# Performance work log

Hardware: AMD Instinct MI355X
Metric: run time of the kernel (lower is better)

Reference implementation:

```python
import jax, jax.numpy as jnp
import numpy as np

K = 10
ALPHA = 0.1
BETA = 0.9
GAMMA = BETA ** K + ALPHA * sum(BETA ** i for i in range(K))


def setup_inputs() -> dict:
    key = jax.random.key(0)
    k1, k2, k3 = jax.random.split(key, 3)
    N, D, E = 100000, 256, 1600000
    x = jax.random.normal(k1, (N, D), dtype=jnp.float32)
    edge_weight = jax.random.uniform(k2, (E,), dtype=jnp.float32)
    edge_index = jax.random.randint(k3, (2, E), 0, N, dtype=jnp.int32)
    return {"x": x, "edge_weight": edge_weight, "edge_index": edge_index}


def reference(x, edge_weight, edge_index):
    N = x.shape[0]
    # gcn_norm_adj with renorm: add self-loops (weight 1) then D^-1/2 A D^-1/2
    loops = jnp.arange(N, dtype=edge_index.dtype)
    row = jnp.concatenate([edge_index[0], loops])
    col = jnp.concatenate([edge_index[1], loops])
    w = jnp.concatenate([edge_weight, jnp.ones((N,), dtype=x.dtype)])
    deg = jax.ops.segment_sum(w, row, num_segments=N)
    dinv = jnp.where(deg > 0, jax.lax.rsqrt(deg), 0.0)
    wn = dinv[row] * w * dinv[col]  # normalized edge weights [E+N]

    h = x
    out = h
    for _ in range(K):
        # SpMM: out[r] = sum_e wn[e] * out[col[e]] for row[e]==r
        msg = wn[:, None] * out[col]
        out = jax.ops.segment_sum(msg, row, num_segments=N)
        out = out * BETA + h * ALPHA
    out = out / GAMMA
    return out
```

## Files before the change

### kernel.cpp

```cpp
#include <hip/hip_runtime.h>
#include <hip/hip_fp16.h>
#include <math.h>

#define DFEAT 256
#define KITER 10
#define ALPHA 0.1f
#define BETA 0.9f
#define SCAN_CHUNK 2048


__global__ void count_deg_kernel(const int* __restrict__ row,
                                 const float* __restrict__ w,
                                 float* __restrict__ deg,
                                 int* __restrict__ counts, int E) {
    int e = blockIdx.x * 256 + threadIdx.x;
    if (e < E) {
        int r = row[e];
        atomicAdd(&deg[r], w[e]);
        atomicAdd(&counts[r], 1);
    }
}

__global__ void dinv_kernel(float* __restrict__ deg, int n) {
    int i = blockIdx.x * 256 + threadIdx.x;
    if (i < n) deg[i] = rsqrtf(deg[i] + 1.0f);
}


__global__ __launch_bounds__(256) void scan1_kernel(const int* __restrict__ counts,
                                                    int* __restrict__ row_ptr,
                                                    int* __restrict__ partial, int n) {
    __shared__ int wsum[4];
    int b = blockIdx.x;
    int base = b * SCAN_CHUNK;
    int tid = threadIdx.x;
    int lane = tid & 63, wv = tid >> 6;

    int v[8];
    int s = 0;
    #pragma unroll
    for (int j = 0; j < 8; ++j) {
        int i = base + tid * 8 + j;
        v[j] = (i < n) ? counts[i] : 0;
        s += v[j];
    }
    int incl = s;
    #pragma unroll
    for (int off = 1; off < 64; off <<= 1) {
        int t = __shfl_up(incl, off, 64);
        if (lane >= off) incl += t;
    }
    if (lane == 63) wsum[wv] = incl;
    __syncthreads();
    int woff = 0;
    for (int w = 0; w < wv; ++w) woff += wsum[w];
    int run = woff + incl - s;
    #pragma unroll
    for (int j = 0; j < 8; ++j) {
        int i = base + tid * 8 + j;
        if (i < n) row_ptr[i] = run;
        run += v[j];
    }
    if (tid == 255) partial[b] = run;
}

__global__ void scan2_kernel(int* __restrict__ partial, int nb) {
    __shared__ int tmp[1024];
    int tid = threadIdx.x;
    int v = (tid < nb) ? partial[tid] : 0;
    tmp[tid] = v;
    __syncthreads();
    for (int off = 1; off < 1024; off <<= 1) {
        int t = (tid >= off) ? tmp[tid - off] : 0;
        __syncthreads();
        tmp[tid] += t;
        __syncthreads();
    }
    if (tid < nb) partial[tid] = tmp[tid] - v;
}

__global__ void scan3_kernel(int* __restrict__ row_ptr, int* __restrict__ fill,
                             const int* __restrict__ partial, int n, int E) {
    int i = blockIdx.x * 256 + threadIdx.x;
    if (i < n) {
        int v = row_ptr[i] + partial[i / SCAN_CHUNK];
        row_ptr[i] = v;
        fill[i] = v;
    } else if (i == n) {
        row_ptr[n] = E;
    }
}

__global__ void scatter_kernel(const int* __restrict__ row, const int* __restrict__ col,
                               const float* __restrict__ w, const float* __restrict__ dinv,
                               int* __restrict__ fill, int2* __restrict__ cw, int E) {
    int e = blockIdx.x * 256 + threadIdx.x;
    if (e < E) {
        int r = row[e], c = col[e];
        float wn = dinv[r] * w[e] * dinv[c];
        int pos = atomicAdd(&fill[r], 1);
        cw[pos] = make_int2(c, __float_as_int(wn));
    }
}

__global__ void f2h_kernel(const float* __restrict__ src, __half* __restrict__ dst,
                           size_t n4) {
    size_t i = (size_t)blockIdx.x * 256 + threadIdx.x;
    if (i < n4) {
        float4 v = ((const float4*)src)[i];
        __half2 h0 = __floats2half2_rn(v.x, v.y);
        __half2 h1 = __floats2half2_rn(v.z, v.w);
        float2 o;
        o.x = *reinterpret_cast<float*>(&h0);
        o.y = *reinterpret_cast<float*>(&h1);
        ((float2*)dst)[i] = o;
    }
}

#define ACC(g, wbits) { float wv = __int_as_float(wbits); \
    __half2 h0_ = *reinterpret_cast<__half2*>(&g.x); \
    __half2 h1_ = *reinterpret_cast<__half2*>(&g.y); \
    float2 u0_ = __half22float2(h0_); float2 u1_ = __half22float2(h1_); \
    a0 += wv * u0_.x; a1 += wv * u0_.y; a2 += wv * u1_.x; a3 += wv * u1_.y; }

template<int FINAL>
__global__ __launch_bounds__(256) void spmm_h_kernel(
        const __half* __restrict__ in, const __half* __restrict__ xh,
        float* __restrict__ outf, __half* __restrict__ outh,
        const int* __restrict__ row_ptr, const int2* __restrict__ cw,
        const float* __restrict__ dinv,
        int n, float scale) {
    int wave = threadIdx.x >> 6;
    int lane = threadIdx.x & 63;
    int r = blockIdx.x * 4 + wave;
    if (r >= n) return;

    int start = row_ptr[r];
    int end   = row_ptr[r + 1];
    float dr  = dinv[r];
    float ws  = dr * dr;

    float2 xraw = ((const float2*)(xh + (size_t)r * DFEAT))[lane];

    float2 sraw = ((const float2*)(in + (size_t)r * DFEAT))[lane];
    __half2 s0 = *reinterpret_cast<__half2*>(&sraw.x);
    __half2 s1 = *reinterpret_cast<__half2*>(&sraw.y);
    float2 sf0 = __half22float2(s0), sf1 = __half22float2(s1);
    float a0 = ws * sf0.x, a1 = ws * sf0.y, a2 = ws * sf1.x, a3 = ws * sf1.y;

    int e = start;
    for (; e + 4 <= end; e += 4) {
        int2 p0 = cw[e];
        int2 p1 = cw[e + 1];
        int2 p2 = cw[e + 2];
        int2 p3 = cw[e + 3];
        float2 g0 = ((const float2*)(in + (size_t)p0.x * DFEAT))[lane];
        float2 g1 = ((const float2*)(in + (size_t)p1.x * DFEAT))[lane];
        float2 g2 = ((const float2*)(in + (size_t)p2.x * DFEAT))[lane];
        float2 g3 = ((const float2*)(in + (size_t)p3.x * DFEAT))[lane];
        ACC(g0, p0.y);
        ACC(g1, p1.y);
        ACC(g2, p2.y);
        ACC(g3, p3.y);
    }
    for (; e < end; ++e) {
        int2 p = cw[e];
        float2 g = ((const float2*)(in + (size_t)p.x * DFEAT))[lane];
        ACC(g, p.y);
    }

    __half2 x0 = *reinterpret_cast<__half2*>(&xraw.x);
    __half2 x1 = *reinterpret_cast<__half2*>(&xraw.y);
    float2 xf0 = __half22float2(x0), xf1 = __half22float2(x1);
    float o0 = scale * (BETA * a0 + ALPHA * xf0.x);
    float o1 = scale * (BETA * a1 + ALPHA * xf0.y);
    float o2 = scale * (BETA * a2 + ALPHA * xf1.x);
    float o3 = scale * (BETA * a3 + ALPHA * xf1.y);

    if (FINAL) {
        ((float4*)(outf + (size_t)r * DFEAT))[lane] = make_float4(o0, o1, o2, o3);
    } else {
        __half2 h0 = __floats2half2_rn(o0, o1);
        __half2 h1 = __floats2half2_rn(o2, o3);
        float2 o;
        o.x = *reinterpret_cast<float*>(&h0);
        o.y = *reinterpret_cast<float*>(&h1);
        ((float2*)(outh + (size_t)r * DFEAT))[lane] = o;
    }
}


extern "C" void kernel_launch(void* const* d_in, const int* in_sizes, int n_in,
                              void* d_out, int out_size, void* d_ws, size_t ws_size,
                              hipStream_t stream) {
    const float* x  = (const float*)d_in[0];
    const float* ew = (const float*)d_in[1];
    const int*   ei = (const int*)d_in[2];
    int n = in_sizes[0] / DFEAT;
    int E = in_sizes[1];
    const int* row = ei;
    const int* col = ei + E;
    float* out = (float*)d_out;

    char* ws = (char*)d_ws;
    auto alloc = [&](size_t bytes) {
        char* p = ws;
        ws += (bytes + 255) & ~(size_t)255;
        return p;
    };
    float*  deg     = (float*)alloc((size_t)n * 4);
    int*    counts  = (int*)  alloc((size_t)n * 4);
    int*    row_ptr = (int*)  alloc((size_t)(n + 1) * 4);
    int*    fill    = (int*)  alloc((size_t)n * 4);
    int*    partial = (int*)  alloc((size_t)1024 * 4);
    int2*   cw      = (int2*) alloc((size_t)E * 8);
    __half* xh      = (__half*)alloc((size_t)n * DFEAT * 2);
    __half* H0      = (__half*)alloc((size_t)n * DFEAT * 2);
    __half* H1      = (__half*)d_out;

    hipMemsetAsync(deg, 0, (size_t)n * 4, stream);
    hipMemsetAsync(counts, 0, (size_t)n * 4, stream);

    count_deg_kernel<<<(E + 255) / 256, 256, 0, stream>>>(row, ew, deg, counts, E);
    dinv_kernel<<<(n + 255) / 256, 256, 0, stream>>>(deg, n);

    int nb = (n + SCAN_CHUNK - 1) / SCAN_CHUNK;
    scan1_kernel<<<nb, 256, 0, stream>>>(counts, row_ptr, partial, n);
    scan2_kernel<<<1, 1024, 0, stream>>>(partial, nb);
    scan3_kernel<<<(n + 256) / 256, 256, 0, stream>>>(row_ptr, fill, partial, n, E);

    scatter_kernel<<<(E + 255) / 256, 256, 0, stream>>>(row, col, ew, deg, fill, cw, E);

    size_t n4 = (size_t)n * DFEAT / 4;
    f2h_kernel<<<(int)((n4 + 255) / 256), 256, 0, stream>>>(x, xh, n4);

    double gamma = pow((double)BETA, KITER);
    for (int i = 0; i < KITER; ++i) gamma += (double)ALPHA * pow((double)BETA, i);
    float inv_gamma = (float)(1.0 / gamma);

    int grid = (n + 3) / 4;
    const __half* cur = xh;
    __half* bufs[2] = { H0, H1 };
    for (int k = 0; k < KITER; ++k) {
        if (k < KITER - 1) {
            __half* o = bufs[k & 1];
            spmm_h_kernel<0><<<grid, 256, 0, stream>>>(cur, xh, nullptr, o,
                                                       row_ptr, cw, deg, n, 1.0f);
            cur = o;
        } else {
            spmm_h_kernel<1><<<grid, 256, 0, stream>>>(cur, xh, out, nullptr,
                                                       row_ptr, cw, deg, n, inv_gamma);
        }
    }
}
```

Before: 1.555 ms.

## Pack degree and count atomics, precompute edge ranks, fold normalization into features

A single 64-bit atomic now accumulates both the edge count (upper bits) and a fixed-point weighted degree (lower bits) per row. The value it returns gives each edge its rank within the row, so the CSR scatter no longer needs a second atomic pass or gathers of dinv. The symmetric normalization moves into the feature vectors: the iterate is carried as D^-1/2 times the output, so CSR stores raw edge weights and the scaling by dinv is undone once at the end. The costs are an extra rank array of E ints and fixed-point rounding of the degree sums.

Measured after the change: 1.447 ms. -6.9%, faster.

```diff
diff --git a/kernel.cpp b/kernel.cpp
--- a/kernel.cpp
+++ b/kernel.cpp
@@ -8,26 +8,36 @@
 #define BETA 0.9f
 #define SCAN_CHUNK 2048
 
-
-__global__ void count_deg_kernel(const int* __restrict__ row,
-                                 const float* __restrict__ w,
-                                 float* __restrict__ deg,
-                                 int* __restrict__ counts, int E) {
+#define WSCALE 268435456.0
+#define CNT_SHIFT 40
+
+
+__global__ void edge_pass1_kernel(const int* __restrict__ row,
+                                  const float* __restrict__ w,
+                                  unsigned long long* __restrict__ pk,
+                                  int* __restrict__ rank, int E) {
     int e = blockIdx.x * 256 + threadIdx.x;
     if (e < E) {
         int r = row[e];
-        atomicAdd(&deg[r], w[e]);
-        atomicAdd(&counts[r], 1);
-    }
-}
-
-__global__ void dinv_kernel(float* __restrict__ deg, int n) {
+        unsigned long long add = (1ULL << CNT_SHIFT) |
+            (unsigned long long)((double)w[e] * WSCALE);
+        unsigned long long old = atomicAdd(&pk[r], add);
+        rank[e] = (int)(old >> CNT_SHIFT);
+    }
+}
+
+__global__ void dinv_kernel(const unsigned long long* __restrict__ pk,
+                            float* __restrict__ dinv, int n) {
     int i = blockIdx.x * 256 + threadIdx.x;
-    if (i < n) deg[i] = rsqrtf(deg[i] + 1.0f);
-}
-
-
-__global__ __launch_bounds__(256) void scan1_kernel(const int* __restrict__ counts,
+    if (i < n) {
+        unsigned long long v = pk[i];
+        float deg = (float)((double)(v & ((1ULL << CNT_SHIFT) - 1)) * (1.0 / WSCALE));
+        dinv[i] = rsqrtf(deg + 1.0f);
+    }
+}
+
+
+__global__ __launch_bounds__(256) void scan1_kernel(const unsigned long long* __restrict__ pk,
                                                     int* __restrict__ row_ptr,
                                                     int* __restrict__ partial, int n) {
     __shared__ int wsum[4];
@@ -41,7 +51,7 @@
     #pragma unroll
     for (int j = 0; j < 8; ++j) {
         int i = base + tid * 8 + j;
-        v[j] = (i < n) ? counts[i] : 0;
+        v[j] = (i < n) ? (int)(pk[i] >> CNT_SHIFT) : 0;
         s += v[j];
     }
     int incl = s;
@@ -79,37 +89,36 @@
     if (tid < nb) partial[tid] = tmp[tid] - v;
 }
 
-__global__ void scan3_kernel(int* __restrict__ row_ptr, int* __restrict__ fill,
+__global__ void scan3_kernel(int* __restrict__ row_ptr,
                              const int* __restrict__ partial, int n, int E) {
     int i = blockIdx.x * 256 + threadIdx.x;
     if (i < n) {
-        int v = row_ptr[i] + partial[i / SCAN_CHUNK];
-        row_ptr[i] = v;
-        fill[i] = v;
+        row_ptr[i] += partial[i / SCAN_CHUNK];
     } else if (i == n) {
         row_ptr[n] = E;
     }
 }
 
 __global__ void scatter_kernel(const int* __restrict__ row, const int* __restrict__ col,
-                               const float* __restrict__ w, const float* __restrict__ dinv,
-                               int* __restrict__ fill, int2* __restrict__ cw, int E) {
+                               const float* __restrict__ w, const int* __restrict__ rank,
+                               const int* __restrict__ row_ptr,
+                               int2* __restrict__ cw, int E) {
     int e = blockIdx.x * 256 + threadIdx.x;
     if (e < E) {
-        int r = row[e], c = col[e];
-        float wn = dinv[r] * w[e] * dinv[c];
-        int pos = atomicAdd(&fill[r], 1);
-        cw[pos] = make_int2(c, __float_as_int(wn));
-    }
-}
-
-__global__ void f2h_kernel(const float* __restrict__ src, __half* __restrict__ dst,
-                           size_t n4) {
+        int r = row[e];
+        int pos = row_ptr[r] + rank[e];
+        cw[pos] = make_int2(col[e], __float_as_int(w[e]));
+    }
+}
+
+__global__ void xprime_kernel(const float* __restrict__ x, const float* __restrict__ dinv,
+                              __half* __restrict__ dst, size_t n4) {
     size_t i = (size_t)blockIdx.x * 256 + threadIdx.x;
     if (i < n4) {
-        float4 v = ((const float4*)src)[i];
-        __half2 h0 = __floats2half2_rn(v.x, v.y);
-        __half2 h1 = __floats2half2_rn(v.z, v.w);
+        float4 v = ((const float4*)x)[i];
+        float dr = dinv[i >> 6];
+        __half2 h0 = __floats2half2_rn(dr * v.x, dr * v.y);
+        __half2 h1 = __floats2half2_rn(dr * v.z, dr * v.w);
         float2 o;
         o.x = *reinterpret_cast<float*>(&h0);
         o.y = *reinterpret_cast<float*>(&h1);
@@ -129,7 +138,7 @@
         float* __restrict__ outf, __half* __restrict__ outh,
         const int* __restrict__ row_ptr, const int2* __restrict__ cw,
         const float* __restrict__ dinv,
-        int n, float scale) {
+        int n, float inv_gamma) {
     int wave = threadIdx.x >> 6;
     int lane = threadIdx.x & 63;
     int r = blockIdx.x * 4 + wave;
@@ -138,7 +147,7 @@
     int start = row_ptr[r];
     int end   = row_ptr[r + 1];
     float dr  = dinv[r];
-    float ws  = dr * dr;
+    float c1  = BETA * dr * dr;
 
     float2 xraw = ((const float2*)(xh + (size_t)r * DFEAT))[lane];
 
@@ -146,7 +155,7 @@
     __half2 s0 = *reinterpret_cast<__half2*>(&sraw.x);
     __half2 s1 = *reinterpret_cast<__half2*>(&sraw.y);
     float2 sf0 = __half22float2(s0), sf1 = __half22float2(s1);
-    float a0 = ws * sf0.x, a1 = ws * sf0.y, a2 = ws * sf1.x, a3 = ws * sf1.y;
+    float a0 = sf0.x, a1 = sf0.y, a2 = sf1.x, a3 = sf1.y;
 
     int e = start;
     for (; e + 4 <= end; e += 4) {
@@ -172,13 +181,15 @@
     __half2 x0 = *reinterpret_cast<__half2*>(&xraw.x);
     __half2 x1 = *reinterpret_cast<__half2*>(&xraw.y);
     float2 xf0 = __half22float2(x0), xf1 = __half22float2(x1);
-    float o0 = scale * (BETA * a0 + ALPHA * xf0.x);
-    float o1 = scale * (BETA * a1 + ALPHA * xf0.y);
-    float o2 = scale * (BETA * a2 + ALPHA * xf1.x);
-    float o3 = scale * (BETA * a3 + ALPHA * xf1.y);
+    float o0 = c1 * a0 + ALPHA * xf0.x;
+    float o1 = c1 * a1 + ALPHA * xf0.y;
+    float o2 = c1 * a2 + ALPHA * xf1.x;
+    float o3 = c1 * a3 + ALPHA * xf1.y;
 
     if (FINAL) {
-        ((float4*)(outf + (size_t)r * DFEAT))[lane] = make_float4(o0, o1, o2, o3);
+        float up = inv_gamma / dr;
+        ((float4*)(outf + (size_t)r * DFEAT))[lane] =
+            make_float4(o0 * up, o1 * up, o2 * up, o3 * up);
     } else {
         __half2 h0 = __floats2half2_rn(o0, o1);
         __half2 h1 = __floats2half2_rn(o2, o3);
@@ -208,31 +219,30 @@
         ws += (bytes + 255) & ~(size_t)255;
         return p;
     };
-    float*  deg     = (float*)alloc((size_t)n * 4);
-    int*    counts  = (int*)  alloc((size_t)n * 4);
+    unsigned long long* pk = (unsigned long long*)alloc((size_t)n * 8);
+    int*    rank    = (int*)  alloc((size_t)E * 4);
     int*    row_ptr = (int*)  alloc((size_t)(n + 1) * 4);
-    int*    fill    = (int*)  alloc((size_t)n * 4);
     int*    partial = (int*)  alloc((size_t)1024 * 4);
+    float*  dinv    = (float*)alloc((size_t)n * 4);
     int2*   cw      = (int2*) alloc((size_t)E * 8);
     __half* xh      = (__half*)alloc((size_t)n * DFEAT * 2);
     __half* H0      = (__half*)alloc((size_t)n * DFEAT * 2);
     __half* H1      = (__half*)d_out;
 
-    hipMemsetAsync(deg, 0, (size_t)n * 4, stream);
-    hipMemsetAsync(counts, 0, (size_t)n * 4, stream);
-
-    count_deg_kernel<<<(E + 255) / 256, 256, 0, stream>>>(row, ew, deg, counts, E);
-    dinv_kernel<<<(n + 255) / 256, 256, 0, stream>>>(deg, n);
+    hipMemsetAsync(pk, 0, (size_t)n * 8, stream);
+
+    edge_pass1_kernel<<<(E + 255) / 256, 256, 0, stream>>>(row, ew, pk, rank, E);
+    dinv_kernel<<<(n + 255) / 256, 256, 0, stream>>>(pk, dinv, n);
 
     int nb = (n + SCAN_CHUNK - 1) / SCAN_CHUNK;
-    scan1_kernel<<<nb, 256, 0, stream>>>(counts, row_ptr, partial, n);
+    scan1_kernel<<<nb, 256, 0, stream>>>(pk, row_ptr, partial, n);
     scan2_kernel<<<1, 1024, 0, stream>>>(partial, nb);
-    scan3_kernel<<<(n + 256) / 256, 256, 0, stream>>>(row_ptr, fill, partial, n, E);
-
-    scatter_kernel<<<(E + 255) / 256, 256, 0, stream>>>(row, col, ew, deg, fill, cw, E);
+    scan3_kernel<<<(n + 256) / 256, 256, 0, stream>>>(row_ptr, partial, n, E);
+
+    scatter_kernel<<<(E + 255) / 256, 256, 0, stream>>>(row, col, ew, rank, row_ptr, cw, E);
 
     size_t n4 = (size_t)n * DFEAT / 4;
-    f2h_kernel<<<(int)((n4 + 255) / 256), 256, 0, stream>>>(x, xh, n4);
+    xprime_kernel<<<(int)((n4 + 255) / 256), 256, 0, stream>>>(x, dinv, xh, n4);
 
     double gamma = pow((double)BETA, KITER);
     for (int i = 0; i < KITER; ++i) gamma += (double)ALPHA * pow((double)BETA, i);
@@ -245,11 +255,11 @@
         if (k < KITER - 1) {
             __half* o = bufs[k & 1];
             spmm_h_kernel<0><<<grid, 256, 0, stream>>>(cur, xh, nullptr, o,
-                                                       row_ptr, cw, deg, n, 1.0f);
+                                                       row_ptr, cw, dinv, n, 1.0f);
             cur = o;
         } else {
             spmm_h_kernel<1><<<grid, 256, 0, stream>>>(cur, xh, out, nullptr,
-                                                       row_ptr, cw, deg, n, inv_gamma);
+                                                       row_ptr, cw, dinv, n, inv_gamma);
         }
     }
 }
```
